# Optimization experiments

Hardware: AMD Instinct MI355X
Metric: run time of the kernel (lower is better)

Reference implementation:

```python
import jax, jax.numpy as jnp
from jax import lax
import numpy as np

B, P, G, C = 16, 6000, 128, 10
PC_MIN = np.array([-54.0, -54.0, -5.0], np.float32)
PC_MAX = np.array([54.0, 54.0, 3.0], np.float32)
CENTER_RADIUS = 1.5
CANDIDATE_TOPK = 5
NUM_HEADS = 6
CLS_W, ALPHA, GAMMA = 2.0, 0.25, 2.0
REG_W, IOU_W = 0.25, 0.25
EPS = 1e-12
INF1, INF2 = 10000.0, 100000.0


def _aabb(boxes):
    # boxes: (N,7) [cx,cy,cz,dx,dy,dz,yaw] -> AABB (min,max) of the 8 rotated corners
    c, d, yaw = boxes[:, :3], boxes[:, 3:6], boxes[:, 6]
    ca, sa = jnp.abs(jnp.cos(yaw)), jnp.abs(jnp.sin(yaw))
    hx = 0.5 * (d[:, 0] * ca + d[:, 1] * sa)
    hy = 0.5 * (d[:, 0] * sa + d[:, 1] * ca)
    h = jnp.stack([hx, hy, 0.5 * d[:, 2]], -1)
    return c - h, c + h


def _iou3d(pred7, gt7):
    # axis-aligned 3D IoU over corner AABBs (reference stand-in for rotated BboxOverlaps3D)
    pmin, pmax = _aabb(pred7)
    gmin, gmax = _aabb(gt7)
    lo = jnp.maximum(pmin[:, None], gmin[None])   # (P,G,3)
    hi = jnp.minimum(pmax[:, None], gmax[None])
    inter = jnp.prod(jnp.maximum(hi - lo, 0.0), -1)
    vp = jnp.prod(pmax - pmin, -1)
    vg = jnp.prod(gmax - gmin, -1)
    return inter / (vp[:, None] + vg[None] - inter + 1e-7)


def _cost_matrix(pred_logits, pred_boxes, gt_boxes, gt_labels):
    # --- focal classification cost ---
    p = jax.nn.sigmoid(pred_logits)                                  # (P,C)
    neg = -jnp.log(1.0 - p + EPS) * (1.0 - ALPHA) * p ** GAMMA
    pos = -jnp.log(p + EPS) * ALPHA * (1.0 - p) ** GAMMA
    cls_cost = (pos - neg)[:, gt_labels] * CLS_W                     # (P,G)

    gt_norm = jnp.concatenate([gt_boxes[:, :3], jnp.log(gt_boxes[:, 3:6]),
                               jnp.sin(gt_boxes[:, 6:7]), jnp.cos(gt_boxes[:, 6:7])], -1)  # (G,8)
    reg_cost = jnp.abs(pred_boxes[:, None, :8] - gt_norm[None]).sum(-1) * REG_W

    # --- IoU cost on denormalized pred boxes ---
    yaw = jnp.arctan2(pred_boxes[:, 6], pred_boxes[:, 7])
    pred7 = jnp.concatenate([pred_boxes[:, :3], jnp.exp(pred_boxes[:, 3:6]), yaw[:, None]], -1)
    ious = _iou3d(pred7, gt_boxes)                                   # (P,G)
    iou_cost = -ious * IOU_W

    # --- in-gt-box / in-center geometric prior ---
    ctr = pred_boxes[:, :3]
    gmin, gmax = _aabb(gt_boxes)
    in_box = jnp.all((ctr[:, None] > gmin[None]) & (ctr[:, None] < gmax[None]), -1)  # (P,G)
    gc, gd = gt_boxes[:, :3], gt_boxes[:, 3:6]
    lo = gc - CENTER_RADIUS * gd
    hi = gc + CENTER_RADIUS * gd
    in_ctr = jnp.all((ctr[:, None] > lo[None]) & (ctr[:, None] < hi[None]), -1)
    valid = jnp.any(in_box, 1) | jnp.any(in_ctr, 1)                  # (P,)
    in_both = in_box & in_ctr

    cost = cls_cost + reg_cost + iou_cost + (~in_both).astype(cls_cost.dtype) * 100.0
    cost = cost + (~valid).astype(cls_cost.dtype)[:, None] * INF1
    return cost, ious, valid


def _assign(pred_logits, pred_boxes, gt_boxes, gt_labels, head_idx):
    cost, ious, valid = _cost_matrix(pred_logits, pred_boxes, gt_boxes, gt_labels)

    # dynamic-k per gt: sum of top-k ious minus head-schedule offset, truncated, min 1
    k = min(CANDIDATE_TOPK, P)
    topk_ious = lax.top_k(ious.T, k)[0]                              # (G,k)
    dyn = jnp.maximum((topk_ious.sum(1) - 0.5 * (NUM_HEADS - head_idx)).astype(jnp.int32), 1)

    # per-gt lowest-cost top-dyn selection via double argsort ranks
    ranks = jnp.argsort(jnp.argsort(cost, axis=0), axis=0)           # (P,G)
    matching = (ranks < dyn[None, :]).astype(cost.dtype)

    # priors matched to >1 gt: keep only the min-cost gt
    prior_mask = matching.sum(1) > 1
    onehot_min = jax.nn.one_hot(jnp.argmin(cost, 1), G, dtype=cost.dtype)
    matching = jnp.where(prior_mask[:, None], onehot_min, matching)

    rows = jnp.arange(P)

    def cond(s):
        i, cst, m = s
        return jnp.any(m.sum(0) == 0) & (i < G + 8)

    def body(s):
        i, cst, m = s
        cst = cst + (m.sum(1) > 0).astype(cst.dtype)[:, None] * INF2
        unmatched = m.sum(0) == 0                                    # (G,)
        pos = jnp.argmin(cst, 0)                                     # (G,) best prior per gt
        m = jnp.where((rows[:, None] == pos[None]) & unmatched[None], 1.0, m)
        over = jnp.any(m.sum(1) > 1)
        oh = jax.nn.one_hot(jnp.argmin(cst, 1), G, dtype=cst.dtype)
        m = jnp.where(over & prior_mask[:, None], oh, m)             # stale mask, as in torch source
        return i + 1, cst, m

    _, _, matching = lax.while_loop(cond, body, (jnp.int32(0), cost, matching))

    fg = matching.sum(1) > 0                                         # (P,) foreground mask
    matched = jnp.where(fg, jnp.argmax(matching, 1), -1).astype(jnp.int32)
    return fg, matched


def setup_inputs():
    key = jax.random.key(0)
    k1, k2, k3, k4, k5, k6, k7, k8 = jax.random.split(key, 8)
    pred_logits = jax.random.normal(k1, (B, P, C), jnp.float32)
    ctr = jax.random.uniform(k2, (B, P, 3), jnp.float32, jnp.array(PC_MIN), jnp.array(PC_MAX))
    logsz = jnp.log(jax.random.uniform(k3, (B, P, 3), jnp.float32, 1.0, 4.0))
    ang = jax.random.uniform(k4, (B, P, 1), jnp.float32, -np.pi, np.pi)
    vel = jax.random.normal(k5, (B, P, 2), jnp.float32)
    pred_boxes = jnp.concatenate([ctr, logsz, jnp.sin(ang), jnp.cos(ang), vel], -1)
    gctr = jax.random.uniform(k6, (B, G, 3), jnp.float32, jnp.array(PC_MIN), jnp.array(PC_MAX))
    gsz = jax.random.uniform(k7, (B, G, 3), jnp.float32, 1.0, 5.0)
    gyaw = jax.random.uniform(k8, (B, G, 1), jnp.float32, -np.pi, np.pi)
    gt_boxes = jnp.concatenate([gctr, gsz, gyaw], -1)
    gt_labels = jax.random.randint(jax.random.fold_in(key, 99), (B, G), 0, C)
    return {"pred_logits": pred_logits, "pred_boxes": pred_boxes,
            "gt_boxes": gt_boxes, "gt_labels": gt_labels, "head_idx": 5}


def reference(pred_logits, pred_boxes, gt_boxes, gt_labels, head_idx):
    f = lambda pl, pb, gb, gl: _assign(pl, pb, gb, gl, head_idx)
    fg, matched = jax.vmap(f)(pred_logits, pred_boxes, gt_boxes, gt_labels)
    return fg, matched
```

## Files before the change

### kernel.cpp

```cpp
#include <hip/hip_runtime.h>
#include <stdint.h>
#include <math.h>

#define NB 16
#define NP 6000
#define NG 128
#define NC 10
#define SELMAX 4
#define GSTR 24
#define PCH 1024
#define NCH 6
#define CPB 2
#define EPIW 128

typedef unsigned long long u64;
#define NBPs ((size_t)NB * NP)

__device__ __forceinline__ uint32_t fkey(float f) {
  uint32_t u = __float_as_uint(f);
  return (u & 0x80000000u) ? ~u : (u | 0x80000000u);
}
__device__ __forceinline__ float fkey_inv(uint32_t k) {
  uint32_t u = (k & 0x80000000u) ? (k & 0x7fffffffu) : ~k;
  return __uint_as_float(u);
}
__device__ __forceinline__ u64 shfl_xor_u64(u64 v, int m) {
  uint32_t lo = (uint32_t)v, hi = (uint32_t)(v >> 32);
  lo = (uint32_t)__shfl_xor((int)lo, m, 64);
  hi = (uint32_t)__shfl_xor((int)hi, m, 64);
  return ((u64)hi << 32) | lo;
}
__device__ __forceinline__ u64 block_min_u64(u64 v, u64* sred, int lane, int wid) {
  for (int o = 1; o < 64; o <<= 1) {
    u64 t = shfl_xor_u64(v, o);
    if (t < v) v = t;
  }
  __syncthreads();
  if (lane == 0) sred[wid] = v;
  __syncthreads();
  u64 r = sred[0];
  if (sred[1] < r) r = sred[1];
  if (sred[2] < r) r = sred[2];
  if (sred[3] < r) r = sred[3];
  return r;
}

__global__ void prep_gt_kernel(const float* __restrict__ gt_boxes,
                               const int* __restrict__ gt_labels,
                               float* __restrict__ gtaux,
                               int* __restrict__ colcnt,
                               int* __restrict__ wcount) {
#pragma clang fp contract(off)
  int b = blockIdx.x, g = threadIdx.x;
  if (b == 0 && g == 0) wcount[0] = 0;
  if (g >= NG) return;
  const float* gb = gt_boxes + ((size_t)b * NG + g) * 7;
  float cx = gb[0], cy = gb[1], cz = gb[2];
  float dx = gb[3], dy = gb[4], dz = gb[5];
  float yaw = gb[6];
  float cyw = cosf(yaw), syw = sinf(yaw);
  float ca = fabsf(cyw), sa = fabsf(syw);
  float hx = 0.5f * (dx * ca + dy * sa);
  float hy = 0.5f * (dx * sa + dy * ca);
  float hz = 0.5f * dz;
  float gmin0 = cx - hx, gmin1 = cy - hy, gmin2 = cz - hz;
  float gmax0 = cx + hx, gmax1 = cy + hy, gmax2 = cz + hz;
  float vg = ((gmax0 - gmin0) * (gmax1 - gmin1)) * (gmax2 - gmin2);
  float* o = gtaux + ((size_t)b * NG + g) * GSTR;
  o[0] = gmin0; o[1] = gmin1; o[2] = gmin2;
  o[3] = gmax0; o[4] = gmax1; o[5] = gmax2;
  o[6] = cx - 1.5f * dx; o[7] = cy - 1.5f * dy; o[8] = cz - 1.5f * dz;
  o[9] = cx + 1.5f * dx; o[10] = cy + 1.5f * dy; o[11] = cz + 1.5f * dz;
  o[12] = cx; o[13] = cy; o[14] = cz;
  o[15] = logf(dx); o[16] = logf(dy); o[17] = logf(dz);
  o[18] = syw; o[19] = cyw;
  o[20] = vg;
  o[21] = __int_as_float(gt_labels[(size_t)b * NG + g]);
  o[22] = 0.0f; o[23] = 0.0f;
  colcnt[b * NG + g] = 0;
}

__global__ __launch_bounds__(256) void prep_pred_kernel(
    const float* __restrict__ pred_logits,
    const float* __restrict__ pred_boxes,
    const float* __restrict__ gtaux,
    float* __restrict__ paux,
    float* __restrict__ clst,
    int* __restrict__ rowcnt,
    int* __restrict__ rowassign) {
#pragma clang fp contract(off)
  __shared__ float shg[NG * 12];
  const int b = blockIdx.y, tid = threadIdx.x;
  for (int j = tid; j < NG * 12; j += 256) {
    int g = j / 12, k = j % 12;
    shg[j] = gtaux[((size_t)b * NG + g) * GSTR + k];
  }
  __syncthreads();
  const int p = blockIdx.x * 256 + tid;
  if (p >= NP) return;
  const size_t idx = (size_t)b * NP + p;
  const float* lg = pred_logits + idx * NC;
  for (int c = 0; c < NC; ++c) {
    float x = lg[c];
    float pr = 1.0f / (1.0f + expf(-x));
    float neg = (-logf(1.0f - pr + 1e-12f) * 0.75f) * (pr * pr);
    float pos = (-logf(pr + 1e-12f) * 0.25f) * ((1.0f - pr) * (1.0f - pr));
    clst[(size_t)c * NBPs + idx] = (pos - neg) * 2.0f;
  }
  const float* bx = pred_boxes + idx * 10;
  float b0 = bx[0], b1 = bx[1], b2 = bx[2], b3 = bx[3], b4 = bx[4];
  float b5 = bx[5], b6 = bx[6], b7 = bx[7];
  float yaw = atan2f(b6, b7);
  float d0 = expf(b3), d1 = expf(b4), d2 = expf(b5);
  float ca = fabsf(cosf(yaw)), sa = fabsf(sinf(yaw));
  float hx = 0.5f * (d0 * ca + d1 * sa);
  float hy = 0.5f * (d0 * sa + d1 * ca);
  float hz = 0.5f * d2;
  float pmin0 = b0 - hx, pmin1 = b1 - hy, pmin2 = b2 - hz;
  float pmax0 = b0 + hx, pmax1 = b1 + hy, pmax2 = b2 + hz;
  int valid = 0;
  for (int g = 0; g < NG; ++g) {
    const float* s = &shg[g * 12];
    bool inb = (b0 > s[0]) && (b0 < s[3]) && (b1 > s[1]) && (b1 < s[4]) &&
               (b2 > s[2]) && (b2 < s[5]);
    bool inc = (b0 > s[6]) && (b0 < s[9]) && (b1 > s[7]) && (b1 < s[10]) &&
               (b2 > s[8]) && (b2 < s[11]);
    if (inb || inc) { valid = 1; break; }
  }
  float* o = paux + idx * 16;
  o[0] = b0; o[1] = b1; o[2] = b2; o[3] = b3;
  o[4] = b4; o[5] = b5; o[6] = b6; o[7] = b7;
  o[8] = pmin0; o[9] = pmin1; o[10] = pmin2;
  o[11] = pmax0; o[12] = pmax1; o[13] = pmax2;
  o[14] = ((pmax0 - pmin0) * (pmax1 - pmin1)) * (pmax2 - pmin2);
  o[15] = valid ? 0.0f : 10000.0f;
  rowcnt[idx] = 0;
  rowassign[idx] = 0x7fffffff;
}

struct GTp {
  float gmin0, gmin1, gmin2, gmax0, gmax1, gmax2;
  float lo0, lo1, lo2, hi0, hi1, hi2;
  float gtn0, gtn1, gtn2, gtn3, gtn4, gtn5, gtn6, gtn7;
  float vg;
  int label;
};
__device__ __forceinline__ GTp load_gt(const float* __restrict__ gtaux,
                                       int b, int g) {
  const float* ga = gtaux + ((size_t)b * NG + g) * GSTR;
  GTp t;
  t.gmin0 = ga[0]; t.gmin1 = ga[1]; t.gmin2 = ga[2];
  t.gmax0 = ga[3]; t.gmax1 = ga[4]; t.gmax2 = ga[5];
  t.lo0 = ga[6]; t.lo1 = ga[7]; t.lo2 = ga[8];
  t.hi0 = ga[9]; t.hi1 = ga[10]; t.hi2 = ga[11];
  t.gtn0 = ga[12]; t.gtn1 = ga[13]; t.gtn2 = ga[14]; t.gtn3 = ga[15];
  t.gtn4 = ga[16]; t.gtn5 = ga[17]; t.gtn6 = ga[18]; t.gtn7 = ga[19];
  t.vg = ga[20];
  t.label = __float_as_int(ga[21]);
  return t;
}

__device__ __forceinline__ float cost_base(
    float b0, float b1, float b2, float b3, float b4, float b5, float b6,
    float b7, float pmin0, float pmin1, float pmin2, float pmax0, float pmax1,
    float pmax2, float vp, float cls, const GTp& t, float* iou_out) {
#pragma clang fp contract(off)
  float r = fabsf(b0 - t.gtn0);
  r = r + fabsf(b1 - t.gtn1);
  r = r + fabsf(b2 - t.gtn2);
  r = r + fabsf(b3 - t.gtn3);
  r = r + fabsf(b4 - t.gtn4);
  r = r + fabsf(b5 - t.gtn5);
  r = r + fabsf(b6 - t.gtn6);
  r = r + fabsf(b7 - t.gtn7);
  float reg = r * 0.25f;
  float li0 = fmaxf(pmin0, t.gmin0), li1 = fmaxf(pmin1, t.gmin1),
        li2 = fmaxf(pmin2, t.gmin2);
  float hj0 = fminf(pmax0, t.gmax0), hj1 = fminf(pmax1, t.gmax1),
        hj2 = fminf(pmax2, t.gmax2);
  float e0 = fmaxf(hj0 - li0, 0.0f), e1 = fmaxf(hj1 - li1, 0.0f),
        e2 = fmaxf(hj2 - li2, 0.0f);
  float inter = (e0 * e1) * e2;
  float iou = inter / (((vp + t.vg) - inter) + 1e-7f);
  bool inb = (b0 > t.gmin0) && (b0 < t.gmax0) && (b1 > t.gmin1) &&
             (b1 < t.gmax1) && (b2 > t.gmin2) && (b2 < t.gmax2);
  bool inc = (b0 > t.lo0) && (b0 < t.hi0) && (b1 > t.lo1) && (b1 < t.hi1) &&
             (b2 > t.lo2) && (b2 < t.hi2);
  *iou_out = iou;
  return ((cls + reg) + (-(iou * 0.25f))) + ((inb && inc) ? 0.0f : 100.0f);
}

__global__ __launch_bounds__(256) void stage1_kernel(
    const float* __restrict__ paux,
    const float* __restrict__ clst,
    const float* __restrict__ gtaux,
    float* __restrict__ iou5,
    u64* __restrict__ ck) {
#pragma clang fp contract(off)
  const int n = blockIdx.x;
  const int orig = (n & 7) * 768 + (n >> 3);
  const int b = orig / 384;
  const int rem = orig - b * 384;
  const int gq = rem / NCH;
  const int ch = rem - gq * NCH;
  const int g0 = gq * CPB;
  const int tid = threadIdx.x;
  const int lane = tid & 63, wid = tid >> 6;

  __shared__ uint32_t kiouL[CPB][PCH];
  __shared__ uint32_t kcostL[CPB][PCH];

  GTp t0 = load_gt(gtaux, b, g0);
  GTp t1 = load_gt(gtaux, b, g0 + 1);
  const size_t rowbase = (size_t)b * NP;
  const uint32_t PAD_I = fkey(-INFINITY);
  const uint32_t PAD_C = fkey(INFINITY);

  for (int j = 0; j < 4; ++j) {
    const int pl = j * 256 + tid;
    const int p = ch * PCH + pl;
    uint32_t ki0 = PAD_I, ki1 = PAD_I, kc0 = PAD_C, kc1 = PAD_C;
    if (p < NP) {
      const size_t idx = rowbase + p;
      const float4* pa = (const float4*)(paux + idx * 16);
      float4 A = pa[0], B = pa[1], C = pa[2], D = pa[3];
      float cls0 = clst[(size_t)t0.label * NBPs + idx];
      float cls1 = clst[(size_t)t1.label * NBPs + idx];
      float iou0, iou1;
      float c0 = cost_base(A.x, A.y, A.z, A.w, B.x, B.y, B.z, B.w,
                           C.x, C.y, C.z, C.w, D.x, D.y, D.z,
                           cls0, t0, &iou0);
      float c1 = cost_base(A.x, A.y, A.z, A.w, B.x, B.y, B.z, B.w,
                           C.x, C.y, C.z, C.w, D.x, D.y, D.z,
                           cls1, t1, &iou1);
      ki0 = fkey(iou0); kc0 = fkey(c0 + D.w);
      ki1 = fkey(iou1); kc1 = fkey(c1 + D.w);
    }
    kiouL[0][pl] = ki0;
    kiouL[1][pl] = ki1;
    kcostL[0][pl] = kc0;
    kcostL[1][pl] = kc1;
  }
  __syncthreads();

  const int c = wid >> 1;
  const int col = b * NG + g0 + c;
  const unsigned gbase = (unsigned)(ch * PCH);

  if ((wid & 1) == 0) {
    u64 last = ~0ull;
    for (int k = 0; k < 5; ++k) {
      u64 best = 0;
      for (int q = 0; q < 16; ++q) {
        const int pl = q * 64 + lane;
        u64 key = ((u64)kiouL[c][pl] << 32) | (u64)(gbase + (unsigned)pl);
        if (key < last && key > best) best = key;
      }
      for (int o = 1; o < 64; o <<= 1) {
        u64 t = shfl_xor_u64(best, o);
        if (t > best) best = t;
      }
      if (lane == 0)
        iou5[(size_t)col * 32 + ch * 5 + k] = fkey_inv((uint32_t)(best >> 32));
      last = best;
    }
  } else {
    u64 last = 0;
    for (int k = 0; k < 4; ++k) {
      u64 best = ~0ull;
      for (int q = 0; q < 16; ++q) {
        const int pl = q * 64 + lane;
        u64 key = ((u64)kcostL[c][pl] << 32) | (u64)(gbase + (unsigned)pl);
        if (key > last && key < best) best = key;
      }
      for (int o = 1; o < 64; o <<= 1) {
        u64 t = shfl_xor_u64(best, o);
        if (t < best) best = t;
      }
      if (lane == 0) ck[(size_t)col * 32 + ch * 4 + k] = best;
      last = best;
    }
  }
}

__global__ __launch_bounds__(256) void stage2_kernel(
    const float* __restrict__ iou5,
    const u64* __restrict__ ck,
    const int* __restrict__ head_ptr,
    int* __restrict__ colsel,
    int* __restrict__ rowcnt,
    int* __restrict__ rowassign,
    int* __restrict__ wlist,
    int* __restrict__ wcount) {
#pragma clang fp contract(off)
  const int col = blockIdx.x * 256 + threadIdx.x;
  if (col >= NB * NG) return;
  const int b = col / NG, g = col - b * NG;
  const float* ip = iou5 + (size_t)col * 32;
  float m0 = -INFINITY, m1 = -INFINITY, m2 = -INFINITY, m3 = -INFINITY,
        m4 = -INFINITY;
  for (int i = 0; i < 5 * NCH; ++i) {
    float v = ip[i];
    if (v > m4) {
      m4 = v;
      if (m4 > m3) { float t = m4; m4 = m3; m3 = t; }
      if (m3 > m2) { float t = m3; m3 = m2; m2 = t; }
      if (m2 > m1) { float t = m2; m2 = m1; m1 = t; }
      if (m1 > m0) { float t = m1; m1 = m0; m0 = t; }
    }
  }
  float sum5 = ((((m0 + m1) + m2) + m3) + m4);
  float adj = sum5 - 0.5f * (float)(6 - head_ptr[0]);
  int dyn = (int)adj;
  if (dyn < 1) dyn = 1;
  if (dyn > SELMAX) dyn = SELMAX;

  const u64* kp = ck + (size_t)col * 32;
  u64 s0 = ~0ull, s1 = ~0ull, s2 = ~0ull, s3 = ~0ull;
  for (int i = 0; i < SELMAX * NCH; ++i) {
    u64 k = kp[i];
    if (k < s3) {
      s3 = k;
      if (s3 < s2) { u64 t = s3; s3 = s2; s2 = t; }
      if (s2 < s1) { u64 t = s2; s2 = s1; s1 = t; }
      if (s1 < s0) { u64 t = s1; s1 = s0; s0 = t; }
    }
  }
  const size_t rowbase = (size_t)b * NP;
  int pk[4];
  pk[0] = (int)(s0 & 0xffffffffu);
  pk[1] = (int)(s1 & 0xffffffffu);
  pk[2] = (int)(s2 & 0xffffffffu);
  pk[3] = (int)(s3 & 0xffffffffu);
  for (int k = 0; k < SELMAX; ++k) {
    int sel = (k < dyn) ? pk[k] : -1;
    colsel[(size_t)col * SELMAX + k] = sel;
    if (sel >= 0) {
      int old = atomicAdd(&rowcnt[rowbase + sel], 1);
      if (old == 1) {
        int slot = atomicAdd(wcount, 1);
        wlist[slot] = (int)(rowbase + sel);
      }
      atomicMin(&rowassign[rowbase + sel], g);
    }
  }
}

__global__ __launch_bounds__(256) void epi_kernel(
    const float* __restrict__ paux,
    const float* __restrict__ clst,
    const float* __restrict__ gtaux,
    const int* __restrict__ colsel,
    const int* __restrict__ rowcnt,
    const int* __restrict__ wlist,
    const int* __restrict__ wcount,
    int* __restrict__ rowminArr,
    int* __restrict__ colcnt) {
#pragma clang fp contract(off)
  const int tid = threadIdx.x;
  if (blockIdx.x >= EPIW) {
    const int col = (blockIdx.x - EPIW) * 256 + tid;
    if (col < NB * NG) {
      const int b = col / NG;
      int cnt = 0;
      const size_t cb = (size_t)col * SELMAX;
      for (int k = 0; k < SELMAX; ++k) {
        int s = colsel[cb + k];
        if (s >= 0 && rowcnt[(size_t)b * NP + s] == 1) cnt++;
      }
      if (cnt) atomicAdd(&colcnt[col], cnt);
    }
    return;
  }
  const int lane = tid & 63, wid = tid >> 6;
  const int wavesTotal = EPIW * 4;
  const int wave = blockIdx.x * 4 + wid;
  const int n = wcount[0];
  for (int e = wave; e < n; e += wavesTotal) {
    const int idx = wlist[e];
    const int b = idx / NP;
    const float4* pa = (const float4*)(paux + (size_t)idx * 16);
    float4 A = pa[0], Bq = pa[1], Cq = pa[2], Dq = pa[3];
    const float pen = Dq.w;
    u64 best = ~0ull;
    for (int h = 0; h < 2; ++h) {
      const int g = h * 64 + lane;
      GTp t = load_gt(gtaux, b, g);
      float cls = clst[(size_t)t.label * NBPs + idx];
      float iou;
      float cc = cost_base(A.x, A.y, A.z, A.w, Bq.x, Bq.y, Bq.z, Bq.w,
                           Cq.x, Cq.y, Cq.z, Cq.w, Dq.x, Dq.y, Dq.z,
                           cls, t, &iou);
      u64 key = ((u64)fkey(cc + pen) << 32) | (unsigned)g;
      if (key < best) best = key;
    }
    for (int o = 1; o < 64; o <<= 1) {
      u64 t = shfl_xor_u64(best, o);
      if (t < best) best = t;
    }
    if (lane == 0) {
      const int bg = (int)(best & 0xffffffffu);
      rowminArr[idx] = bg;
      atomicAdd(&colcnt[b * NG + bg], 1);
    }
  }
}

__global__ __launch_bounds__(256) void fixup_kernel(
    const float* __restrict__ paux,
    const float* __restrict__ clst,
    const float* __restrict__ gtaux,
    const int* __restrict__ colcnt,
    const int* __restrict__ rowcnt,
    int* __restrict__ rowassign) {
#pragma clang fp contract(off)
  const int g = blockIdx.x, b = blockIdx.y, tid = threadIdx.x;
  if (colcnt[b * NG + g] != 0) return;
  const int lane = tid & 63, wid = tid >> 6;
  const size_t rowbase = (size_t)b * NP;
  GTp t = load_gt(gtaux, b, g);
  u64 best = ~0ull;
  for (int p = tid; p < NP; p += 256) {
    const size_t idx = rowbase + p;
    if (rowcnt[idx] == 0) {
      const float4* pa = (const float4*)(paux + idx * 16);
      float4 A = pa[0], Bq = pa[1], Cq = pa[2], Dq = pa[3];
      float cls = clst[(size_t)t.label * NBPs + idx];
      float iou;
      float cc = cost_base(A.x, A.y, A.z, A.w, Bq.x, Bq.y, Bq.z, Bq.w,
                           Cq.x, Cq.y, Cq.z, Cq.w, Dq.x, Dq.y, Dq.z,
                           cls, t, &iou);
      u64 key = ((u64)fkey(cc + Dq.w) << 32) | (unsigned)p;
      if (key < best) best = key;
    }
  }
  __shared__ u64 sred[4];
  u64 rr = block_min_u64(best, sred, lane, wid);
  if (tid == 0) {
    int pos = (int)(rr & 0xffffffffu);
    atomicMin(&rowassign[rowbase + pos], g);
  }
}

__global__ void output_kernel(const int* __restrict__ rowcnt,
                              const int* __restrict__ rowassign,
                              const int* __restrict__ rowminArr,
                              int* __restrict__ out) {
  const int i = blockIdx.x * 256 + threadIdx.x;
  if (i >= (int)NBPs) return;
  int rc = rowcnt[i];
  int fg, m;
  if (rc == 0) {
    int ra = rowassign[i];
    if (ra == 0x7fffffff) { fg = 0; m = -1; }
    else { fg = 1; m = ra; }
  } else if (rc == 1) {
    fg = 1; m = rowassign[i];
  } else {
    fg = 1; m = rowminArr[i];
  }
  out[i] = fg;
  out[NBPs + i] = m;
}

extern "C" void kernel_launch(void* const* d_in, const int* in_sizes, int n_in,
                              void* d_out, int out_size, void* d_ws, size_t ws_size,
                              hipStream_t stream) {
  const float* pred_logits = (const float*)d_in[0];
  const float* pred_boxes = (const float*)d_in[1];
  const float* gt_boxes = (const float*)d_in[2];
  const int* gt_labels = (const int*)d_in[3];
  const int* head = (const int*)d_in[4];
  (void)in_sizes; (void)n_in; (void)out_size; (void)ws_size;

  char* w = (char*)d_ws;
  size_t off = 0;
  auto alloc = [&](size_t bytes) -> void* {
    void* p = w + off;
    off += (bytes + 255) & ~(size_t)255;
    return p;
  };
  float* paux = (float*)alloc((size_t)NB * NP * 16 * 4);
  float* clst = (float*)alloc((size_t)NC * NB * NP * 4);
  float* gtaux = (float*)alloc((size_t)NB * NG * GSTR * 4);
  float* iou5 = (float*)alloc((size_t)NB * NG * 32 * 4);
  u64* ck = (u64*)alloc((size_t)NB * NG * 32 * 8);
  int* colsel = (int*)alloc((size_t)NB * NG * SELMAX * 4);
  int* rowcnt = (int*)alloc((size_t)NB * NP * 4);
  int* rowassign = (int*)alloc((size_t)NB * NP * 4);
  int* rowminArr = (int*)alloc((size_t)NB * NP * 4);
  int* colcnt = (int*)alloc((size_t)NB * NG * 4);
  int* wlist = (int*)alloc((size_t)NB * NP * 4);
  int* wcount = (int*)alloc(256);

  int* out = (int*)d_out;
  dim3 blk(256);
  prep_gt_kernel<<<dim3(NB), dim3(128), 0, stream>>>(
      gt_boxes, gt_labels, gtaux, colcnt, wcount);
  prep_pred_kernel<<<dim3((NP + 255) / 256, NB), blk, 0, stream>>>(
      pred_logits, pred_boxes, gtaux, paux, clst, rowcnt, rowassign);
  stage1_kernel<<<dim3(NB * (NG / CPB) * NCH), blk, 0, stream>>>(
      paux, clst, gtaux, iou5, ck);
  stage2_kernel<<<dim3((NB * NG + 255) / 256), blk, 0, stream>>>(
      iou5, ck, head, colsel, rowcnt, rowassign, wlist, wcount);
  epi_kernel<<<dim3(EPIW + 8), blk, 0, stream>>>(
      paux, clst, gtaux, colsel, rowcnt, wlist, wcount, rowminArr, colcnt);
  fixup_kernel<<<dim3(NG, NB), blk, 0, stream>>>(
      paux, clst, gtaux, colcnt, rowcnt, rowassign);
  output_kernel<<<dim3(((int)NBPs + 255) / 256), blk, 0, stream>>>(
      rowcnt, rowassign, rowminArr, out);
}
```

Before: 135.8 us.

## Fuse GT prep into pred prep and use per-lane top-k with larger chunks

Merges the GT preprocessing kernel into the pred preprocessing kernel, so each block recomputes GT AABB data into shared memory and block x=0 writes gtaux. This removes one launch and a global round-trip. The stage1 chunk grows from 1024 to 2048 preds (3 chunks instead of 6), which halves the number of blocks and partial candidates. The repeated full-scan selection is replaced by a per-lane register top-k followed by wave-level merge rounds. The cost is fewer blocks for occupancy and more register pressure from the sorted lists.

```diff
diff --git a/kernel.cpp b/kernel.cpp
--- a/kernel.cpp
+++ b/kernel.cpp
@@ -8,9 +8,10 @@
 #define NC 10
 #define SELMAX 4
 #define GSTR 24
-#define PCH 1024
-#define NCH 6
+#define PCH 2048
+#define NCH 3
 #define CPB 2
+#define QITER 32
 #define EPIW 128
 
 typedef unsigned long long u64;
@@ -45,55 +46,55 @@
   return r;
 }
 
-__global__ void prep_gt_kernel(const float* __restrict__ gt_boxes,
-                               const int* __restrict__ gt_labels,
-                               float* __restrict__ gtaux,
-                               int* __restrict__ colcnt,
-                               int* __restrict__ wcount) {
-#pragma clang fp contract(off)
-  int b = blockIdx.x, g = threadIdx.x;
-  if (b == 0 && g == 0) wcount[0] = 0;
-  if (g >= NG) return;
-  const float* gb = gt_boxes + ((size_t)b * NG + g) * 7;
-  float cx = gb[0], cy = gb[1], cz = gb[2];
-  float dx = gb[3], dy = gb[4], dz = gb[5];
-  float yaw = gb[6];
-  float cyw = cosf(yaw), syw = sinf(yaw);
-  float ca = fabsf(cyw), sa = fabsf(syw);
-  float hx = 0.5f * (dx * ca + dy * sa);
-  float hy = 0.5f * (dx * sa + dy * ca);
-  float hz = 0.5f * dz;
-  float gmin0 = cx - hx, gmin1 = cy - hy, gmin2 = cz - hz;
-  float gmax0 = cx + hx, gmax1 = cy + hy, gmax2 = cz + hz;
-  float vg = ((gmax0 - gmin0) * (gmax1 - gmin1)) * (gmax2 - gmin2);
-  float* o = gtaux + ((size_t)b * NG + g) * GSTR;
-  o[0] = gmin0; o[1] = gmin1; o[2] = gmin2;
-  o[3] = gmax0; o[4] = gmax1; o[5] = gmax2;
-  o[6] = cx - 1.5f * dx; o[7] = cy - 1.5f * dy; o[8] = cz - 1.5f * dz;
-  o[9] = cx + 1.5f * dx; o[10] = cy + 1.5f * dy; o[11] = cz + 1.5f * dz;
-  o[12] = cx; o[13] = cy; o[14] = cz;
-  o[15] = logf(dx); o[16] = logf(dy); o[17] = logf(dz);
-  o[18] = syw; o[19] = cyw;
-  o[20] = vg;
-  o[21] = __int_as_float(gt_labels[(size_t)b * NG + g]);
-  o[22] = 0.0f; o[23] = 0.0f;
-  colcnt[b * NG + g] = 0;
-}
-
-__global__ __launch_bounds__(256) void prep_pred_kernel(
+__global__ __launch_bounds__(256) void prep_kernel(
+    const float* __restrict__ gt_boxes,
+    const int* __restrict__ gt_labels,
     const float* __restrict__ pred_logits,
     const float* __restrict__ pred_boxes,
-    const float* __restrict__ gtaux,
+    float* __restrict__ gtaux,
     float* __restrict__ paux,
     float* __restrict__ clst,
     int* __restrict__ rowcnt,
-    int* __restrict__ rowassign) {
+    int* __restrict__ rowassign,
+    int* __restrict__ colcnt,
+    int* __restrict__ wcount) {
 #pragma clang fp contract(off)
   __shared__ float shg[NG * 12];
   const int b = blockIdx.y, tid = threadIdx.x;
-  for (int j = tid; j < NG * 12; j += 256) {
-    int g = j / 12, k = j % 12;
-    shg[j] = gtaux[((size_t)b * NG + g) * GSTR + k];
+  if (tid < NG) {
+    const int g = tid;
+    const float* gb = gt_boxes + ((size_t)b * NG + g) * 7;
+    float cx = gb[0], cy = gb[1], cz = gb[2];
+    float dx = gb[3], dy = gb[4], dz = gb[5];
+    float yaw = gb[6];
+    float cyw = cosf(yaw), syw = sinf(yaw);
+    float ca = fabsf(cyw), sa = fabsf(syw);
+    float hx = 0.5f * (dx * ca + dy * sa);
+    float hy = 0.5f * (dx * sa + dy * ca);
+    float hz = 0.5f * dz;
+    float gmin0 = cx - hx, gmin1 = cy - hy, gmin2 = cz - hz;
+    float gmax0 = cx + hx, gmax1 = cy + hy, gmax2 = cz + hz;
+    float* s = &shg[g * 12];
+    s[0] = gmin0; s[1] = gmin1; s[2] = gmin2;
+    s[3] = gmax0; s[4] = gmax1; s[5] = gmax2;
+    s[6] = cx - 1.5f * dx; s[7] = cy - 1.5f * dy; s[8] = cz - 1.5f * dz;
+    s[9] = cx + 1.5f * dx; s[10] = cy + 1.5f * dy; s[11] = cz + 1.5f * dz;
+    if (blockIdx.x == 0) {
+      float vg = ((gmax0 - gmin0) * (gmax1 - gmin1)) * (gmax2 - gmin2);
+      float* o = gtaux + ((size_t)b * NG + g) * GSTR;
+      o[0] = gmin0; o[1] = gmin1; o[2] = gmin2;
+      o[3] = gmax0; o[4] = gmax1; o[5] = gmax2;
+      o[6] = s[6]; o[7] = s[7]; o[8] = s[8];
+      o[9] = s[9]; o[10] = s[10]; o[11] = s[11];
+      o[12] = cx; o[13] = cy; o[14] = cz;
+      o[15] = logf(dx); o[16] = logf(dy); o[17] = logf(dz);
+      o[18] = syw; o[19] = cyw;
+      o[20] = vg;
+      o[21] = __int_as_float(gt_labels[(size_t)b * NG + g]);
+      o[22] = 0.0f; o[23] = 0.0f;
+      colcnt[b * NG + g] = 0;
+      if (b == 0 && g == 0) wcount[0] = 0;
+    }
   }
   __syncthreads();
   const int p = blockIdx.x * 256 + tid;
@@ -198,9 +199,9 @@
     u64* __restrict__ ck) {
 #pragma clang fp contract(off)
   const int n = blockIdx.x;
-  const int orig = (n & 7) * 768 + (n >> 3);
-  const int b = orig / 384;
-  const int rem = orig - b * 384;
+  const int orig = (n & 7) * 384 + (n >> 3);
+  const int b = orig / 192;
+  const int rem = orig - b * 192;
   const int gq = rem / NCH;
   const int ch = rem - gq * NCH;
   const int g0 = gq * CPB;
@@ -216,7 +217,7 @@
   const uint32_t PAD_I = fkey(-INFINITY);
   const uint32_t PAD_C = fkey(INFINITY);
 
-  for (int j = 0; j < 4; ++j) {
+  for (int j = 0; j < PCH / 256; ++j) {
     const int pl = j * 256 + tid;
     const int p = ch * PCH + pl;
     uint32_t ki0 = PAD_I, ki1 = PAD_I, kc0 = PAD_C, kc1 = PAD_C;
@@ -248,37 +249,54 @@
   const unsigned gbase = (unsigned)(ch * PCH);
 
   if ((wid & 1) == 0) {
-    u64 last = ~0ull;
+    uint32_t a0 = 0, a1 = 0, a2 = 0, a3 = 0, a4 = 0;
+    for (int q = 0; q < QITER; ++q) {
+      uint32_t k = kiouL[c][q * 64 + lane];
+      if (k > a4) {
+        a4 = k;
+        if (a4 > a3) { uint32_t t = a4; a4 = a3; a3 = t; }
+        if (a3 > a2) { uint32_t t = a3; a3 = a2; a2 = t; }
+        if (a2 > a1) { uint32_t t = a2; a2 = a1; a1 = t; }
+        if (a1 > a0) { uint32_t t = a1; a1 = a0; a0 = t; }
+      }
+    }
+    int hp = 0;
     for (int k = 0; k < 5; ++k) {
-      u64 best = 0;
-      for (int q = 0; q < 16; ++q) {
-        const int pl = q * 64 + lane;
-        u64 key = ((u64)kiouL[c][pl] << 32) | (u64)(gbase + (unsigned)pl);
-        if (key < last && key > best) best = key;
-      }
+      uint32_t cand = (hp == 0) ? a0 : (hp == 1) ? a1 : (hp == 2) ? a2
+                    : (hp == 3) ? a3 : (hp == 4) ? a4 : 0u;
+      u64 key = ((u64)cand << 32) | (unsigned)lane;
+      u64 r = key;
       for (int o = 1; o < 64; o <<= 1) {
-        u64 t = shfl_xor_u64(best, o);
-        if (t > best) best = t;
+        u64 t = shfl_xor_u64(r, o);
+        if (t > r) r = t;
       }
       if (lane == 0)
-        iou5[(size_t)col * 32 + ch * 5 + k] = fkey_inv((uint32_t)(best >> 32));
-      last = best;
+        iou5[(size_t)col * 16 + ch * 5 + k] = fkey_inv((uint32_t)(r >> 32));
+      if (r == key) hp++;
     }
   } else {
-    u64 last = 0;
+    u64 c0 = ~0ull, c1 = ~0ull, c2 = ~0ull, c3 = ~0ull;
+    for (int q = 0; q < QITER; ++q) {
+      const int pl = q * 64 + lane;
+      u64 key = ((u64)kcostL[c][pl] << 32) | (u64)(gbase + (unsigned)pl);
+      if (key < c3) {
+        c3 = key;
+        if (c3 < c2) { u64 t = c3; c3 = c2; c2 = t; }
+        if (c2 < c1) { u64 t = c2; c2 = c1; c1 = t; }
+        if (c1 < c0) { u64 t = c1; c1 = c0; c0 = t; }
+      }
+    }
+    int hp = 0;
     for (int k = 0; k < 4; ++k) {
-      u64 best = ~0ull;
-      for (int q = 0; q < 16; ++q) {
-        const int pl = q * 64 + lane;
-        u64 key = ((u64)kcostL[c][pl] << 32) | (u64)(gbase + (unsigned)pl);
-        if (key > last && key < best) best = key;
+      u64 cand = (hp == 0) ? c0 : (hp == 1) ? c1 : (hp == 2) ? c2
+               : (hp == 3) ? c3 : ~0ull;
+      u64 r = cand;
+      for (int o = 1; o < 64; o <<= 1) {
+        u64 t = shfl_xor_u64(r, o);
+        if (t < r) r = t;
       }
-      for (int o = 1; o < 64; o <<= 1) {
-        u64 t = shfl_xor_u64(best, o);
-        if (t < best) best = t;
-      }
-      if (lane == 0) ck[(size_t)col * 32 + ch * 4 + k] = best;
-      last = best;
+      if (lane == 0) ck[(size_t)col * 16 + ch * 4 + k] = r;
+      if (r == cand) hp++;
     }
   }
 }
@@ -296,7 +314,7 @@
   const int col = blockIdx.x * 256 + threadIdx.x;
   if (col >= NB * NG) return;
   const int b = col / NG, g = col - b * NG;
-  const float* ip = iou5 + (size_t)col * 32;
+  const float* ip = iou5 + (size_t)col * 16;
   float m0 = -INFINITY, m1 = -INFINITY, m2 = -INFINITY, m3 = -INFINITY,
         m4 = -INFINITY;
   for (int i = 0; i < 5 * NCH; ++i) {
@@ -315,7 +333,7 @@
   if (dyn < 1) dyn = 1;
   if (dyn > SELMAX) dyn = SELMAX;
 
-  const u64* kp = ck + (size_t)col * 32;
+  const u64* kp = ck + (size_t)col * 16;
   u64 s0 = ~0ull, s1 = ~0ull, s2 = ~0ull, s3 = ~0ull;
   for (int i = 0; i < SELMAX * NCH; ++i) {
     u64 k = kp[i];
@@ -483,8 +501,8 @@
   float* paux = (float*)alloc((size_t)NB * NP * 16 * 4);
   float* clst = (float*)alloc((size_t)NC * NB * NP * 4);
   float* gtaux = (float*)alloc((size_t)NB * NG * GSTR * 4);
-  float* iou5 = (float*)alloc((size_t)NB * NG * 32 * 4);
-  u64* ck = (u64*)alloc((size_t)NB * NG * 32 * 8);
+  float* iou5 = (float*)alloc((size_t)NB * NG * 16 * 4);
+  u64* ck = (u64*)alloc((size_t)NB * NG * 16 * 8);
   int* colsel = (int*)alloc((size_t)NB * NG * SELMAX * 4);
   int* rowcnt = (int*)alloc((size_t)NB * NP * 4);
   int* rowassign = (int*)alloc((size_t)NB * NP * 4);
@@ -495,10 +513,9 @@
 
   int* out = (int*)d_out;
   dim3 blk(256);
-  prep_gt_kernel<<<dim3(NB), dim3(128), 0, stream>>>(
-      gt_boxes, gt_labels, gtaux, colcnt, wcount);
-  prep_pred_kernel<<<dim3((NP + 255) / 256, NB), blk, 0, stream>>>(
-      pred_logits, pred_boxes, gtaux, paux, clst, rowcnt, rowassign);
+  prep_kernel<<<dim3((NP + 255) / 256, NB), blk, 0, stream>>>(
+      gt_boxes, gt_labels, pred_logits, pred_boxes, gtaux, paux, clst,
+      rowcnt, rowassign, colcnt, wcount);
   stage1_kernel<<<dim3(NB * (NG / CPB) * NCH), blk, 0, stream>>>(
       paux, clst, gtaux, iou5, ck);
   stage2_kernel<<<dim3((NB * NG + 255) / 256), blk, 0, stream>>>(
```

Result: faster. 123.2 us (-9.3%).
